# Performance work log

Hardware: AMD Instinct MI355X
Metric: run time of the kernel (lower is better)

The kernel has to match this reference:

```python
import jax, jax.numpy as jnp
import numpy as np
from jax import lax

NUM_CNNS = 300
INPUT_LEN = 608
NUM_CLASSES = 50
FILTER = 19
POOL = 7
HIDDEN = 100
BATCH = 256
L_CONV = INPUT_LEN - FILTER + 1          # 590
L_POOL = (L_CONV - POOL) // POOL + 1     # 84
EPS = 1e-5


def setup_inputs() -> dict:
    key = jax.random.key(0)
    ks = jax.random.split(key, 24)
    U, H = NUM_CNNS, HIDDEN
    d = {}
    d["x"] = jax.random.normal(ks[0], (BATCH, 4, INPUT_LEN), dtype=jnp.float32)
    # conv1: grouped Conv1d(4*U -> U, k=19, groups=U) on replicated input == dense Conv1d(4 -> U)
    d["w1"] = jax.random.normal(ks[1], (U, 4, FILTER), dtype=jnp.float32) * 0.1
    d["b1"] = jax.random.normal(ks[2], (U,), dtype=jnp.float32) * 0.05
    d["g1"] = jax.random.uniform(ks[3], (U,), dtype=jnp.float32, minval=0.5, maxval=1.5)
    d["be1"] = jax.random.normal(ks[4], (U,), dtype=jnp.float32) * 0.05
    d["m1"] = jax.random.normal(ks[5], (U,), dtype=jnp.float32) * 0.05
    d["v1"] = jax.random.uniform(ks[6], (U,), dtype=jnp.float32, minval=0.5, maxval=1.5)
    # grouped 1x1 conv: per-unit Linear 84 -> 100
    d["w2"] = jax.random.normal(ks[7], (U, H, L_POOL), dtype=jnp.float32) * (1.0 / np.sqrt(L_POOL))
    d["b2"] = jax.random.normal(ks[8], (U, H), dtype=jnp.float32) * 0.05
    d["g2"] = jax.random.uniform(ks[9], (U, H), dtype=jnp.float32, minval=0.5, maxval=1.5)
    d["be2"] = jax.random.normal(ks[10], (U, H), dtype=jnp.float32) * 0.05
    d["m2"] = jax.random.normal(ks[11], (U, H), dtype=jnp.float32) * 0.05
    d["v2"] = jax.random.uniform(ks[12], (U, H), dtype=jnp.float32, minval=0.5, maxval=1.5)
    # grouped 1x1 conv: per-unit Linear 100 -> 1
    d["w3"] = jax.random.normal(ks[13], (U, H), dtype=jnp.float32) * (1.0 / np.sqrt(H))
    d["b3"] = jax.random.normal(ks[14], (U,), dtype=jnp.float32) * 0.05
    d["g3"] = jax.random.uniform(ks[15], (U,), dtype=jnp.float32, minval=0.5, maxval=1.5)
    d["be3"] = jax.random.normal(ks[16], (U,), dtype=jnp.float32) * 0.05
    d["m3"] = jax.random.normal(ks[17], (U,), dtype=jnp.float32) * 0.05
    d["v3"] = jax.random.uniform(ks[18], (U,), dtype=jnp.float32, minval=0.5, maxval=1.5)
    # final Linear(U -> num_classes)
    d["wf"] = jax.random.normal(ks[19], (NUM_CLASSES, U), dtype=jnp.float32) * (1.0 / np.sqrt(U))
    d["bf"] = jax.random.normal(ks[20], (NUM_CLASSES,), dtype=jnp.float32) * 0.05
    return d


def _bn(y, g, be, m, v):
    return (y - m) * (g * lax.rsqrt(v + EPS)) + be


def reference(x, w1, b1, g1, be1, m1, v1, w2, b2, g2, be2, m2, v2,
              w3, b3, g3, be3, m3, v3, wf, bf):
    # conv1 (replicate + grouped conv == dense conv over 4 channels)
    y = lax.conv_general_dilated(x, w1, window_strides=(1,), padding='VALID',
                                 dimension_numbers=('NCH', 'OIH', 'NCH'))  # [B,U,590]
    y = y + b1[None, :, None]
    y = _bn(y, g1[None, :, None], be1[None, :, None], m1[None, :, None], v1[None, :, None])
    y = jnp.exp(y)  # ExpActivation
    # MaxPool1d(7,7): 590 -> 84 (uses first 588 positions)
    B = y.shape[0]
    y = y[:, :, :L_POOL * POOL].reshape(B, NUM_CNNS, L_POOL, POOL).max(axis=-1)  # [B,U,84]
    # per-unit MLP 84 -> 100 (grouped 1x1 conv) + BN + ReLU (dropout is eval-mode identity)
    h = jnp.einsum('buf,uof->buo', y, w2) + b2[None]  # [B,U,100]
    h = _bn(h, g2[None], be2[None], m2[None], v2[None])
    h = jax.nn.relu(h)
    # per-unit 100 -> 1 + BN + ReLU
    z = jnp.einsum('buo,uo->bu', h, w3) + b3[None]  # [B,U]
    z = _bn(z, g3[None], be3[None], m3[None], v3[None])
    z = jax.nn.relu(z)
    # final Linear
    return z @ wf.T + bf
```

## Files before the change

kernel.cpp:

```cpp
#include <hip/hip_runtime.h>
#include <hip/hip_bf16.h>

#define BATCH    256
#define NU       300
#define LIN      608
#define FILT     19
#define LPOOL    84
#define POOL     7
#define HID      100
#define NCLS     50
#define EPS      1e-5f
#define KP       96
#define NP       112
#define LDK      104
#define WROW     104
#define WBROWS   320
#define TCHUNK   112
#define MTN      19
#define BH       128

typedef __attribute__((ext_vector_type(8))) short short8;
typedef __attribute__((ext_vector_type(4))) float float4v;

#define LDS_WAIT() __asm__ __volatile__("s_waitcnt lgkmcnt(0)" ::: "memory")

__device__ __forceinline__ unsigned short f2bf(float f) {
    unsigned u = __float_as_uint(f);
    u += 0x7fffu + ((u >> 16) & 1u);
    return (unsigned short)(u >> 16);
}
__device__ __forceinline__ float bf2f(unsigned short h) {
    return __uint_as_float(((unsigned)h) << 16);
}

__global__ void k_prep(const float* __restrict__ w1, const float* __restrict__ x,
                       const float* __restrict__ b1, const float* __restrict__ g1,
                       const float* __restrict__ be1, const float* __restrict__ m1,
                       const float* __restrict__ v1,
                       unsigned short* __restrict__ Wbh,
                       unsigned short* __restrict__ Wbl,
                       unsigned int* __restrict__ xc,
                       float2* __restrict__ s1c1)
{
    const int idx = blockIdx.x * 256 + threadIdx.x;
    const int NW = WBROWS * WROW;
    if (idx < NW) {
        const int u = idx / WROW, kk = idx - u * WROW;
        float wv = 0.f;
        if (u < NU && kk < 96) {
            const int c = kk / 24, tap = kk - 24 * c;
            if (tap < FILT) wv = w1[(u * 4 + c) * FILT + tap];
        }
        const unsigned short hi = f2bf(wv);
        Wbh[idx] = hi;
        Wbl[idx] = f2bf(wv - bf2f(hi));
    }
    const int j = idx - NW;
    if (j >= 0 && j < BATCH * 4 * LIN) {
        const float xv = x[j];
        const unsigned short hi = f2bf(xv);
        const unsigned short lo = f2bf(xv - bf2f(hi));
        xc[j] = (unsigned)hi | ((unsigned)lo << 16);
    }
    const int j2 = j - BATCH * 4 * LIN;
    if (j2 >= 0 && j2 < MTN * 16) {
        float2 v = {0.f, 0.f};
        if (j2 < NU) {
            const float s = g1[j2] * rsqrtf(v1[j2] + EPS);
            v.x = s;
            v.y = (b1[j2] - m1[j2]) * s + be1[j2];
        }
        s1c1[j2] = v;
    }
}

__global__ __launch_bounds__(256, 3)
void k_conv7d(const unsigned short* __restrict__ Wbh,
              const unsigned short* __restrict__ Wbl,
              const unsigned int* __restrict__ xc,
              const float2* __restrict__ s1c1,
              unsigned short* __restrict__ ypool)
{
    __shared__ __align__(16) unsigned short Bh[TCHUNK * LDK];
    __shared__ __align__(16) float Cs[4][TCHUNK * 4];

    const int tid = threadIdx.x;
    const int b   = blockIdx.x;
    const int tc  = blockIdx.y;
    const int t0  = TCHUNK * tc;
    const int NT  = (tc == 5) ? 2 : 7;

    for (int i = tid; i < TCHUNK * 12; i += 256) {
        const int trow = i / 12;
        if (trow >= 16 * NT) continue;
        const int rem   = i - 12 * trow;
        const int c     = rem / 3;
        const int third = rem - 3 * c;
        const int kkb   = 24 * c + 8 * third;
        const int tt0   = t0 + trow + 8 * third;
        const unsigned int* src = xc + ((b * 4 + c) * LIN + tt0);

        unsigned int w[8];
        if (third < 2 && tt0 + 8 <= LIN) {
            const uint4 v0 = *(const uint4*)(src);
            const uint4 v1 = *(const uint4*)(src + 4);
            w[0] = v0.x; w[1] = v0.y; w[2] = v0.z; w[3] = v0.w;
            w[4] = v1.x; w[5] = v1.y; w[6] = v1.z; w[7] = v1.w;
        } else {
#pragma unroll
            for (int j = 0; j < 8; ++j) {
                const int tap = 8 * third + j;
                const int tt  = tt0 + j;
                unsigned int v = 0;
                if (tap < FILT && tt < LIN) v = src[j];
                w[j] = v;
            }
        }
        short8 hv;
#pragma unroll
        for (int j = 0; j < 8; ++j) hv[j] = (short)(w[j] & 0xffffu);
        *(short8*)(&Bh[trow * LDK + kkb]) = hv;
    }
    __syncthreads();

    const int lane = tid & 63;
    const int n    = lane & 15;
    const int quad = lane >> 4;
    const int wave = tid >> 6;
    float* Csw = Cs[wave];

    const int ep_ul = lane & 3;
    const int ep_p  = lane >> 2;

    for (int k = wave; k < 10; k += 4) {
        const int mt0 = 2 * k;
        const bool two = (mt0 + 1 < MTN);

        short8 a0h[3], a0l[3], a1h[3], a1l[3];
        {
            const unsigned short* wrh = Wbh + (size_t)(mt0 * 16 + n) * WROW;
            const unsigned short* wrl = Wbl + (size_t)(mt0 * 16 + n) * WROW;
#pragma unroll
            for (int s = 0; s < 3; ++s) {
                a0h[s] = *(const short8*)(wrh + 32 * s + 8 * quad);
                a0l[s] = *(const short8*)(wrl + 32 * s + 8 * quad);
            }
            const int m1r = two ? (mt0 + 1) : mt0;
            const unsigned short* wrh1 = Wbh + (size_t)(m1r * 16 + n) * WROW;
            const unsigned short* wrl1 = Wbl + (size_t)(m1r * 16 + n) * WROW;
#pragma unroll
            for (int s = 0; s < 3; ++s) {
                a1h[s] = *(const short8*)(wrh1 + 32 * s + 8 * quad);
                a1l[s] = *(const short8*)(wrl1 + 32 * s + 8 * quad);
            }
        }

        float4v acc[2][7];
#pragma unroll
        for (int t2 = 0; t2 < 2; ++t2)
#pragma unroll
            for (int nt = 0; nt < 7; ++nt)
                acc[t2][nt] = (float4v){0.f, 0.f, 0.f, 0.f};

#pragma unroll
        for (int nt = 0; nt < 7; ++nt) {
            if (nt < NT) {
                short8 bhf[3];
#pragma unroll
                for (int s = 0; s < 3; ++s)
                    bhf[s] = *(const short8*)(&Bh[(16 * nt + n) * LDK + 32 * s + 8 * quad]);
#pragma unroll
                for (int s = 0; s < 3; ++s)
                    acc[0][nt] = __builtin_amdgcn_mfma_f32_16x16x32_bf16(
                        a0h[s], bhf[s], acc[0][nt], 0, 0, 0);
#pragma unroll
                for (int s = 0; s < 3; ++s)
                    acc[0][nt] = __builtin_amdgcn_mfma_f32_16x16x32_bf16(
                        a0l[s], bhf[s], acc[0][nt], 0, 0, 0);
                if (two) {
#pragma unroll
                    for (int s = 0; s < 3; ++s)
                        acc[1][nt] = __builtin_amdgcn_mfma_f32_16x16x32_bf16(
                            a1h[s], bhf[s], acc[1][nt], 0, 0, 0);
#pragma unroll
                    for (int s = 0; s < 3; ++s)
                        acc[1][nt] = __builtin_amdgcn_mfma_f32_16x16x32_bf16(
                            a1l[s], bhf[s], acc[1][nt], 0, 0, 0);
                }
            }
        }

#pragma unroll
        for (int t2 = 0; t2 < 2; ++t2) {
            if (t2 == 1 && !two) break;
            const int mt = mt0 + t2;
#pragma unroll
            for (int qq = 0; qq < 4; ++qq) {
                LDS_WAIT();
                if (quad == qq) {
#pragma unroll
                    for (int nt = 0; nt < 7; ++nt) {
                        if (nt < NT)
                            *(float4v*)(&Csw[(16 * nt + n) * 4]) = acc[t2][nt];
                    }
                }
                LDS_WAIT();

                const int uglob = mt * 16 + 4 * qq + ep_ul;
                const int pg    = 16 * tc + ep_p;
                if (uglob < NU) {
                    unsigned short outv = 0;
                    if (pg < LPOOL) {
                        float mx = Csw[(7 * ep_p) * 4 + ep_ul];
#pragma unroll
                        for (int j = 1; j < 7; ++j)
                            mx = fmaxf(mx, Csw[(7 * ep_p + j) * 4 + ep_ul]);
                        const float2 sc = s1c1[uglob];
                        outv = f2bf(__expf(fmaf(mx, sc.x, sc.y)));
                    }
                    if (pg < KP)
                        ypool[((size_t)uglob * BATCH + b) * KP + pg] = outv;
                }
            }
        }
    }
}

__global__ __launch_bounds__(256, 3)
void k_mlp(const unsigned short* __restrict__ ypool,
           const float* __restrict__ w2, const float* __restrict__ b2,
           const float* __restrict__ g2, const float* __restrict__ be2,
           const float* __restrict__ m2, const float* __restrict__ v2,
           const float* __restrict__ w3, const float* __restrict__ b3,
           const float* __restrict__ g3, const float* __restrict__ be3,
           const float* __restrict__ m3, const float* __restrict__ v3,
           float* __restrict__ zbuf)
{
    __shared__ __align__(16) unsigned short As[NP * LDK];
    __shared__ __align__(16) unsigned short Bs[BH * LDK];
    __shared__ __align__(16) float4 cs4[NP];

    const int tid = threadIdx.x;
    const int u   = blockIdx.x;
    const int b0  = blockIdx.y * BH;

    {
        const float* src = w2 + (size_t)u * HID * LPOOL;
        for (int c = tid; c < HID * (LPOOL / 4); c += 256) {
            const int o  = c / (LPOOL / 4);
            const int kc = (c % (LPOOL / 4)) * 4;
            const float4 v = *(const float4*)(src + o * LPOOL + kc);
            unsigned short* d = &As[o * LDK + kc];
            d[0] = f2bf(v.x); d[1] = f2bf(v.y); d[2] = f2bf(v.z); d[3] = f2bf(v.w);
        }
        for (int c = tid; c < HID * 6; c += 256) {
            const int o = c / 6, kc = LPOOL + (c % 6) * 2;
            *(unsigned*)(&As[o * LDK + kc]) = 0;
        }
        for (int c = tid; c < (NP - HID) * (KP / 2); c += 256) {
            const int o = HID + c / (KP / 2), kc = (c % (KP / 2)) * 2;
            *(unsigned*)(&As[o * LDK + kc]) = 0;
        }
    }
    {
        const unsigned short* ys = ypool + ((size_t)u * BATCH + b0) * KP;
        for (int c = tid; c < BH * (KP / 8); c += 256) {
            const int n  = c / (KP / 8);
            const int kc = (c % (KP / 8)) * 8;
            *(short8*)(&Bs[n * LDK + kc]) = *(const short8*)(ys + n * KP + kc);
        }
    }
    if (tid < NP) {
        float4 cv = {0.f, 0.f, 0.f, 0.f};
        if (tid < HID) {
            const int uo = u * HID + tid;
            const float s = g2[uo] * rsqrtf(v2[uo] + EPS);
            cv.x = s;
            cv.y = (b2[uo] - m2[uo]) * s + be2[uo];
            cv.z = w3[uo];
        }
        cs4[tid] = cv;
    }
    __syncthreads();

    const int lane = tid & 63;
    const int wave = tid >> 6;
    const int col  = lane & 15;
    const int quad = lane >> 4;

    short8 bf_[2][3];
#pragma unroll
    for (int j = 0; j < 2; ++j) {
        const int brow = 16 * (2 * wave + j) + col;
#pragma unroll
        for (int s = 0; s < 3; ++s)
            bf_[j][s] = *(const short8*)(&Bs[brow * LDK + 32 * s + 8 * quad]);
    }

    float zp0 = 0.f, zp1 = 0.f;
#pragma unroll
    for (int mt = 0; mt < 7; ++mt) {
        short8 af[3];
#pragma unroll
        for (int s = 0; s < 3; ++s)
            af[s] = *(const short8*)(&As[(16 * mt + col) * LDK + 32 * s + 8 * quad]);

        float4v a0 = {0.f, 0.f, 0.f, 0.f}, a1 = {0.f, 0.f, 0.f, 0.f};
#pragma unroll
        for (int s = 0; s < 3; ++s) {
            a0 = __builtin_amdgcn_mfma_f32_16x16x32_bf16(af[s], bf_[0][s], a0, 0, 0, 0);
            a1 = __builtin_amdgcn_mfma_f32_16x16x32_bf16(af[s], bf_[1][s], a1, 0, 0, 0);
        }
#pragma unroll
        for (int r = 0; r < 4; ++r) {
            const float4 cv = cs4[16 * mt + 4 * quad + r];
            zp0 = fmaf(fmaxf(fmaf(a0[r], cv.x, cv.y), 0.f), cv.z, zp0);
            zp1 = fmaf(fmaxf(fmaf(a1[r], cv.x, cv.y), 0.f), cv.z, zp1);
        }
    }

    zp0 += __shfl_xor(zp0, 16); zp0 += __shfl_xor(zp0, 32);
    zp1 += __shfl_xor(zp1, 16); zp1 += __shfl_xor(zp1, 32);

    if (quad == 0) {
        const float s3 = g3[u] * rsqrtf(v3[u] + EPS);
        const float c3 = (b3[u] - m3[u]) * s3 + be3[u];
        const int bA = b0 + 16 * (2 * wave + 0) + col;
        const int bB = b0 + 16 * (2 * wave + 1) + col;
        zbuf[(size_t)u * BATCH + bA] = fmaxf(fmaf(zp0, s3, c3), 0.f);
        zbuf[(size_t)u * BATCH + bB] = fmaxf(fmaf(zp1, s3, c3), 0.f);
    }
}

__global__ __launch_bounds__(256, 4)
void k_final(const float* __restrict__ zbuf, const float* __restrict__ wf,
             const float* __restrict__ bf, float* __restrict__ out)
{
    __shared__ float red[4][64];
    const int nc   = blockIdx.x;
    const int bq   = blockIdx.y;
    const int lane = threadIdx.x & 63;
    const int wave = threadIdx.x >> 6;
    const int b    = bq * 64 + lane;

    float a0 = 0.f, a1 = 0.f, a2 = 0.f;
    const int u0 = wave * 75;
#pragma unroll 5
    for (int i = 0; i < 75; i += 3) {
        a0 = fmaf(zbuf[(size_t)(u0 + i + 0) * BATCH + b], wf[nc * NU + u0 + i + 0], a0);
        a1 = fmaf(zbuf[(size_t)(u0 + i + 1) * BATCH + b], wf[nc * NU + u0 + i + 1], a1);
        a2 = fmaf(zbuf[(size_t)(u0 + i + 2) * BATCH + b], wf[nc * NU + u0 + i + 2], a2);
    }
    red[wave][lane] = (a0 + a1) + a2;
    __syncthreads();
    if (threadIdx.x < 64) {
        const float s = (red[0][lane] + red[1][lane]) + (red[2][lane] + red[3][lane]);
        out[(size_t)b * NCLS + nc] = s + bf[nc];
    }
}

extern "C" void kernel_launch(void* const* d_in, const int* in_sizes, int n_in,
                              void* d_out, int out_size, void* d_ws, size_t ws_size,
                              hipStream_t stream)
{
    const float* x   = (const float*)d_in[0];
    const float* w1  = (const float*)d_in[1];
    const float* b1  = (const float*)d_in[2];
    const float* g1  = (const float*)d_in[3];
    const float* be1 = (const float*)d_in[4];
    const float* m1  = (const float*)d_in[5];
    const float* v1  = (const float*)d_in[6];
    const float* w2  = (const float*)d_in[7];
    const float* b2  = (const float*)d_in[8];
    const float* g2  = (const float*)d_in[9];
    const float* be2 = (const float*)d_in[10];
    const float* m2  = (const float*)d_in[11];
    const float* v2  = (const float*)d_in[12];
    const float* w3  = (const float*)d_in[13];
    const float* b3  = (const float*)d_in[14];
    const float* g3  = (const float*)d_in[15];
    const float* be3 = (const float*)d_in[16];
    const float* m3  = (const float*)d_in[17];
    const float* v3  = (const float*)d_in[18];
    const float* wf  = (const float*)d_in[19];
    const float* bf  = (const float*)d_in[20];

    unsigned short* ypool = (unsigned short*)d_ws;
    float* zbuf = (float*)((char*)d_ws + 14745600);
    unsigned short* Wbh = (unsigned short*)((char*)d_ws + 15052800);
    unsigned short* Wbl = (unsigned short*)((char*)d_ws + 15119360);
    unsigned int*   xc  = (unsigned int*)((char*)d_ws + 15185920);
    float2*         sc1 = (float2*)((char*)d_ws + 17676288);

    const int prep_elems = WBROWS * WROW + BATCH * 4 * LIN + MTN * 16;
    k_prep<<<(prep_elems + 255) / 256, 256, 0, stream>>>(
        w1, x, b1, g1, be1, m1, v1, Wbh, Wbl, xc, sc1);

    dim3 gc(BATCH, 6);
    k_conv7d<<<gc, 256, 0, stream>>>(Wbh, Wbl, xc, sc1, ypool);

    dim3 gm(NU, BATCH / BH);
    k_mlp<<<gm, 256, 0, stream>>>(ypool, w2, b2, g2, be2, m2, v2,
                                  w3, b3, g3, be3, m3, v3, zbuf);

    dim3 gf(NCLS, 4);
    k_final<<<gf, 256, 0, stream>>>(zbuf, wf, bf, (float*)d_out);
}
```

Baseline: 159.3 us.

## Transpose conv MFMA output and stage whole tile once for pooling epilogue

The MFMA operands are swapped so each lane holds four consecutive time positions for one unit. This lets every quad write its full 16x112 tile to padded shared memory in one pass instead of four serialized quad rounds. The wave-to-M-tile assignment becomes contiguous blocks of five tiles per wave instead of strided pairs, which changes load balance. The max-pool reads seven strided values per unit from the padded rows, and the pg<KP guard is dropped because pg never reaches KP here.

Result: faster. 152.7 us (-4.1%).

```diff
diff --git a/kernel.cpp b/kernel.cpp
--- a/kernel.cpp
+++ b/kernel.cpp
@@ -18,6 +18,7 @@
 #define TCHUNK   112
 #define MTN      19
 #define BH       128
+#define CSTR     116
 
 typedef __attribute__((ext_vector_type(8))) short short8;
 typedef __attribute__((ext_vector_type(4))) float float4v;
@@ -82,7 +83,7 @@
               unsigned short* __restrict__ ypool)
 {
     __shared__ __align__(16) unsigned short Bh[TCHUNK * LDK];
-    __shared__ __align__(16) float Cs[4][TCHUNK * 4];
+    __shared__ __align__(16) float Cs[4][16 * CSTR];
 
     const int tid = threadIdx.x;
     const int b   = blockIdx.x;
@@ -129,12 +130,12 @@
     const int wave = tid >> 6;
     float* Csw = Cs[wave];
 
+    const int ep_p  = lane >> 2;
     const int ep_ul = lane & 3;
-    const int ep_p  = lane >> 2;
-
-    for (int k = wave; k < 10; k += 4) {
-        const int mt0 = 2 * k;
-        const bool two = (mt0 + 1 < MTN);
+
+    const int jend = 5 * wave + ((wave == 3) ? 4 : 5);
+    for (int mt0 = 5 * wave; mt0 < jend; mt0 += 2) {
+        const bool two = (mt0 + 1 < jend);
 
         short8 a0h[3], a0l[3], a1h[3], a1l[3];
         {
@@ -172,20 +173,20 @@
 #pragma unroll
                 for (int s = 0; s < 3; ++s)
                     acc[0][nt] = __builtin_amdgcn_mfma_f32_16x16x32_bf16(
-                        a0h[s], bhf[s], acc[0][nt], 0, 0, 0);
+                        bhf[s], a0h[s], acc[0][nt], 0, 0, 0);
 #pragma unroll
                 for (int s = 0; s < 3; ++s)
                     acc[0][nt] = __builtin_amdgcn_mfma_f32_16x16x32_bf16(
-                        a0l[s], bhf[s], acc[0][nt], 0, 0, 0);
+                        bhf[s], a0l[s], acc[0][nt], 0, 0, 0);
                 if (two) {
 #pragma unroll
                     for (int s = 0; s < 3; ++s)
                         acc[1][nt] = __builtin_amdgcn_mfma_f32_16x16x32_bf16(
-                            a1h[s], bhf[s], acc[1][nt], 0, 0, 0);
+                            bhf[s], a1h[s], acc[1][nt], 0, 0, 0);
 #pragma unroll
                     for (int s = 0; s < 3; ++s)
                         acc[1][nt] = __builtin_amdgcn_mfma_f32_16x16x32_bf16(
-                            a1l[s], bhf[s], acc[1][nt], 0, 0, 0);
+                            bhf[s], a1l[s], acc[1][nt], 0, 0, 0);
                 }
             }
         }
@@ -194,32 +195,39 @@
         for (int t2 = 0; t2 < 2; ++t2) {
             if (t2 == 1 && !two) break;
             const int mt = mt0 + t2;
-#pragma unroll
-            for (int qq = 0; qq < 4; ++qq) {
-                LDS_WAIT();
-                if (quad == qq) {
-#pragma unroll
-                    for (int nt = 0; nt < 7; ++nt) {
-                        if (nt < NT)
-                            *(float4v*)(&Csw[(16 * nt + n) * 4]) = acc[t2][nt];
-                    }
+
+            LDS_WAIT();
+#pragma unroll
+            for (int nt = 0; nt < 7; ++nt) {
+                if (nt < NT)
+                    *(float4v*)(&Csw[n * CSTR + 16 * nt + 4 * quad]) = acc[t2][nt];
+            }
+            LDS_WAIT();
+
+            const int  pg  = 16 * tc + ep_p;
+            const bool act = (pg < LPOOL);
+            float mx[4] = {0.f, 0.f, 0.f, 0.f};
+            if (act) {
+#pragma unroll
+                for (int gi = 0; gi < 4; ++gi) {
+                    const float* r = &Csw[(4 * gi + ep_ul) * CSTR + 7 * ep_p];
+                    float m0 = fmaxf(r[0], r[1]);
+                    float m1 = fmaxf(r[2], r[3]);
+                    float m2 = fmaxf(r[4], r[5]);
+                    m0 = fmaxf(m0, r[6]);
+                    mx[gi] = fmaxf(fmaxf(m0, m1), m2);
                 }
-                LDS_WAIT();
-
-                const int uglob = mt * 16 + 4 * qq + ep_ul;
-                const int pg    = 16 * tc + ep_p;
+            }
+#pragma unroll
+            for (int gi = 0; gi < 4; ++gi) {
+                const int uglob = mt * 16 + 4 * gi + ep_ul;
                 if (uglob < NU) {
                     unsigned short outv = 0;
-                    if (pg < LPOOL) {
-                        float mx = Csw[(7 * ep_p) * 4 + ep_ul];
-#pragma unroll
-                        for (int j = 1; j < 7; ++j)
-                            mx = fmaxf(mx, Csw[(7 * ep_p + j) * 4 + ep_ul]);
+                    if (act) {
                         const float2 sc = s1c1[uglob];
-                        outv = f2bf(__expf(fmaf(mx, sc.x, sc.y)));
+                        outv = f2bf(__expf(fmaf(mx[gi], sc.x, sc.y)));
                     }
-                    if (pg < KP)
-                        ypool[((size_t)uglob * BATCH + b) * KP + pg] = outv;
+                    ypool[((size_t)uglob * BATCH + b) * KP + pg] = outv;
                 }
             }
         }
```
